# Performance work log

Measured on AMD Instinct MI355X. Metric: run time of the kernel, lower is better.

## Reference

```python
import jax, jax.numpy as jnp
import numpy as np

D = 1024   # dim_model
H = 16     # num_heads
DH = D // H  # per-head dim for k and v
B, S = 2, 2048
EPS = 1e-5


def layer_norm(x, g, b):
    mu = jnp.mean(x, axis=-1, keepdims=True)
    var = jnp.var(x, axis=-1, keepdims=True)
    return (x - mu) * jax.lax.rsqrt(var + EPS) * g + b


def setup_inputs() -> dict:
    key = jax.random.key(0)
    ks = jax.random.split(key, 8)
    s_d = 1.0 / np.sqrt(D)
    inp = {
        "x": jax.random.normal(ks[0], (B, S, D), dtype=jnp.float32),
        # stacked per-head projections, [H, D, DH] (torch Linear weight.T per head)
        "wq": jax.random.uniform(ks[1], (H, D, DH), jnp.float32, -s_d, s_d),
        "wk": jax.random.uniform(ks[2], (H, D, DH), jnp.float32, -s_d, s_d),
        "wv": jax.random.uniform(ks[3], (H, D, DH), jnp.float32, -s_d, s_d),
        "wo": jax.random.uniform(ks[4], (D, D), jnp.float32, -s_d, s_d),
        "w1": jax.random.uniform(ks[5], (D, D), jnp.float32, -s_d, s_d),  # FFN hidden == dim_model per source
        "w2": jax.random.uniform(ks[6], (D, D), jnp.float32, -s_d, s_d),
        "ln1_g": jnp.ones((D,), jnp.float32), "ln1_b": jnp.zeros((D,), jnp.float32),
        "ln2_g": jnp.ones((D,), jnp.float32), "ln2_b": jnp.zeros((D,), jnp.float32),
        "ln3_g": jnp.ones((D,), jnp.float32), "ln3_b": jnp.zeros((D,), jnp.float32),
    }
    return inp


def reference(x, wq, wk, wv, wo, w1, w2, ln1_g, ln1_b, ln2_g, ln2_b, ln3_g, ln3_b):
    residual = x
    h = layer_norm(x, ln1_g, ln1_b)  # pre_attention_norm
    # batched multi-head attention (equivalent to per-head loop + concat)
    q = jnp.einsum("bsd,hdk->bhsk", h, wq)
    k = jnp.einsum("bsd,hdk->bhsk", h, wk)
    v = jnp.einsum("bsd,hdk->bhsk", h, wv)
    scores = jnp.einsum("bhsk,bhtk->bhst", q, k) / jnp.sqrt(jnp.float32(DH))
    attn = jax.nn.softmax(scores, axis=-1)
    ctx = jnp.einsum("bhst,bhtk->bhsk", attn, v)        # [B,H,S,DH]
    concat = ctx.transpose(0, 2, 1, 3).reshape(x.shape[0], x.shape[1], -1)  # head concat order
    h = concat @ wo
    h = h + residual
    h = layer_norm(h, ln2_g, ln2_b)  # post_attention_norm (dropout is identity, rate=0)
    residual = h
    ffn = jnp.maximum(h @ w1, 0.0) @ w2
    h = ffn + residual
    h = layer_norm(h, ln3_g, ln3_b)  # post_ffn_norm
    return h
```

## Files before the change

### kernel.cpp

```cpp
#include <hip/hip_runtime.h>
#include <stdint.h>

typedef unsigned short u16;
typedef __attribute__((ext_vector_type(8))) short short8;
typedef __attribute__((ext_vector_type(4))) short short4v;
typedef __attribute__((ext_vector_type(4))) float f32x4;

#define DEV static __device__ __forceinline__

constexpr int DMODEL = 1024;
constexpr int SEQ = 2048;

DEV u16 f2b(float f){
  uint32_t u = __float_as_uint(f);
  u += 0x7FFF + ((u >> 16) & 1);
  return (u16)(u >> 16);
}

DEV float b2f(u16 b){ uint32_t u = ((uint32_t)b)<<16; return __uint_as_float(u); }

#define AS1(p) ((const __attribute__((address_space(1))) void*)(p))
#define AS3(p) ((__attribute__((address_space(3))) void*)(p))
#define GLOAD_LDS16(g, l) __builtin_amdgcn_global_load_lds(AS1(g), AS3(l), 16, 0, 0)
#define LDSADDR(p) ((uint32_t)(size_t)((__attribute__((address_space(3))) void*)(p)))

DEV short4v ds_tr16(uint32_t a){
  short4v r;
  asm volatile("ds_read_b64_tr_b16 %0, %1" : "=v"(r) : "v"(a) : "memory");
  return r;
}

DEV void pswap(uint32_t &a, uint32_t &b){
  asm("v_permlane32_swap_b32 %0, %1":"+v"(a),"+v"(b));
  asm("v_permlane16_swap_b32 %0, %1":"+v"(a),"+v"(b));
}

DEV uint32_t cvtpk(float lo, float hi){
  uint32_t r; asm("v_cvt_pk_bf16_f32 %0, %1, %2":"=v"(r):"v"(lo),"v"(hi)); return r;
}

__global__ __launch_bounds__(256) void transpose_all(
    const float* __restrict__ wq, const float* __restrict__ wk,
    const float* __restrict__ wv, const float* __restrict__ wo,
    const float* __restrict__ w1, const float* __restrict__ w2,
    u16* __restrict__ WqkvT, u16* __restrict__ WoT,
    u16* __restrict__ W1T, u16* __restrict__ W2T){
  __shared__ float tile[64][65];
  int bid = blockIdx.x;
  int j = threadIdx.x & 63, i0 = threadIdx.x >> 6;
  if(bid < 768){
    int xb = bid & 15, z = bid >> 4;
    int p = z >> 4, h = z & 15;
    const float* src = (p==0?wq:(p==1?wk:wv)) + (size_t)h*1024*64;
    float sc = (p==0) ? 0.18033688011112042f : 1.0f;
    int r0 = xb*64;
    for(int i=i0;i<64;i+=4) tile[i][j] = src[(size_t)(r0+i)*64 + j];
    __syncthreads();
    u16* drow = WqkvT + ((size_t)p*1024 + h*64)*1024;
    for(int jj=i0;jj<64;jj+=4) drow[(size_t)jj*1024 + r0 + j] = f2b(tile[j][jj]*sc);
  } else {
    int t = bid - 768;
    int which = t >> 8; t &= 255;
    const float* src = which==0?wo:(which==1?w1:w2);
    u16* dst = which==0?WoT:(which==1?W1T:W2T);
    int r0 = (t&15)*64, c0 = (t>>4)*64;
    for(int i=i0;i<64;i+=4) tile[i][j] = src[(size_t)(r0+i)*1024 + c0 + j];
    __syncthreads();
    for(int jj=i0;jj<64;jj+=4) dst[(size_t)(c0+jj)*1024 + r0 + j] = f2b(tile[j][jj]);
  }
}

__global__ __launch_bounds__(256) void ln_kernel(
    const float* __restrict__ in, const float* __restrict__ g, const float* __restrict__ bb,
    u16* __restrict__ outb, float* __restrict__ outf){
  int row = blockIdx.x, tid = threadIdx.x;
  const float4* x4 = (const float4*)(in + (size_t)row*DMODEL);
  float4 v = x4[tid];
  float s  = v.x+v.y+v.z+v.w;
  float ss = v.x*v.x + v.y*v.y + v.z*v.z + v.w*v.w;
  #pragma unroll
  for(int m=1;m<64;m<<=1){ s += __shfl_xor(s,m); ss += __shfl_xor(ss,m); }
  __shared__ float red[8];
  int w = tid>>6;
  if((tid&63)==0){ red[w]=s; red[4+w]=ss; }
  __syncthreads();
  s  = red[0]+red[1]+red[2]+red[3];
  ss = red[4]+red[5]+red[6]+red[7];
  float mu  = s*(1.f/DMODEL);
  float var = ss*(1.f/DMODEL) - mu*mu;
  float rs  = rsqrtf(var + 1e-5f);
  float4 gv = ((const float4*)g)[tid];
  float4 bv = ((const float4*)bb)[tid];
  float y0=(v.x-mu)*rs*gv.x+bv.x, y1=(v.y-mu)*rs*gv.y+bv.y;
  float y2=(v.z-mu)*rs*gv.z+bv.z, y3=(v.w-mu)*rs*gv.w+bv.w;
  if(outb){ ushort4 o = make_ushort4(f2b(y0),f2b(y1),f2b(y2),f2b(y3));
            ((ushort4*)outb)[(size_t)row*(DMODEL/4) + tid] = o; }
  if(outf){ ((float4*)outf)[(size_t)row*(DMODEL/4) + tid] = make_float4(y0,y1,y2,y3); }
}

template<int MODE>
__global__ __launch_bounds__(256) void gemm_bt(
    const u16* __restrict__ A, const u16* __restrict__ BT, int M, int N, int K,
    float* __restrict__ outf, u16* __restrict__ outb, const float* __restrict__ resf,
    const u16* __restrict__ resb){
  __shared__ u16 lsA[2][4096];
  __shared__ u16 lsB[2][4096];
  int n0 = blockIdx.x*128, m0 = blockIdx.y*128;
  int tid = threadIdx.x, lane = tid&63, w = tid>>6;
  int wr = w>>1, wc = w&1, rq = lane&15, hk = lane>>4;
  int o0 = tid*16, o1 = 4096 + tid*16;
  const u16* aS0 = A  + (size_t)(m0 + (o0>>6))*K + ((o0&63)>>1);
  const u16* aS1 = A  + (size_t)(m0 + (o1>>6))*K + ((o1&63)>>1);
  const u16* bS0 = BT + (size_t)(n0 + (o0>>6))*K + ((o0&63)>>1);
  const u16* bS1 = BT + (size_t)(n0 + (o1>>6))*K + ((o1&63)>>1);
  int nk = K>>5;
  f32x4 acc[4][4] = {};
  GLOAD_LDS16(aS0, &lsA[0][w*512]);
  GLOAD_LDS16(aS1, &lsA[0][2048 + w*512]);
  GLOAD_LDS16(bS0, &lsB[0][w*512]);
  GLOAD_LDS16(bS1, &lsB[0][2048 + w*512]);
  #pragma unroll 2
  for(int kt=0; kt<nk; ++kt){
    __syncthreads();
    if(kt+1 < nk){
      int nb = (kt+1)&1;
      GLOAD_LDS16(aS0 + (kt+1)*32, &lsA[nb][w*512]);
      GLOAD_LDS16(aS1 + (kt+1)*32, &lsA[nb][2048 + w*512]);
      GLOAD_LDS16(bS0 + (kt+1)*32, &lsB[nb][w*512]);
      GLOAD_LDS16(bS1 + (kt+1)*32, &lsB[nb][2048 + w*512]);
    }
    const u16* la = &lsA[kt&1][0];
    const u16* lb = &lsB[kt&1][0];
    short8 aF[4], bF[4];
    #pragma unroll
    for(int m=0;m<4;++m) aF[m] = *(const short8*)(la + (wr*64 + m*16 + rq)*32 + hk*8);
    #pragma unroll
    for(int n=0;n<4;++n) bF[n] = *(const short8*)(lb + (wc*64 + n*16 + rq)*32 + hk*8);
    __builtin_amdgcn_s_setprio(1);
    #pragma unroll
    for(int m=0;m<4;++m){
      #pragma unroll
      for(int n=0;n<4;++n)
        acc[m][n] = __builtin_amdgcn_mfma_f32_16x16x32_bf16(aF[m], bF[n], acc[m][n], 0,0,0);
    }
    __builtin_amdgcn_s_setprio(0);
  }
  #pragma unroll
  for(int m=0;m<4;++m){
    #pragma unroll
    for(int n=0;n<4;++n){
      int rb = m0 + wr*64 + m*16 + (hk<<2);
      int c  = n0 + wc*64 + n*16 + rq;
      #pragma unroll
      for(int qq=0;qq<4;++qq){
        int r = rb+qq; float val = acc[m][n][qq];
        if constexpr(MODE==2){
          outf[(size_t)r*N + c] = val + resf[(size_t)r*N + c];
        } else if constexpr(MODE==3){
          outb[(size_t)r*N + c] = f2b(val>0.f?val:0.f);
        } else if constexpr(MODE==4){
          outf[(size_t)r*N + c] = val + b2f(resb[(size_t)r*N + c]);
        } else {
          outb[(size_t)r*N + c] = f2b(val);
        }
      }
    }
  }
}

__global__ __launch_bounds__(128) void attn_kernel(
    const u16* __restrict__ qkv, u16* __restrict__ concat){
  __shared__ u16 lsK[2][4096];
  __shared__ u16 lsV[2][4096];
  int qt = blockIdx.x, bh = blockIdx.y;
  int b = bh>>4, h = bh&15;
  const u16* qp = qkv + (size_t)b*2048*3072 + h*64;
  const u16* kp = qp + 1024;
  const u16* vp = qp + 2048;
  int tid=threadIdx.x, lane=tid&63, w=tid>>6;
  int rq = lane&15, hk = lane>>4;
  const uint32_t sw = (uint32_t)((rq&7)<<4);

  short8 aQ[2][2];
  #pragma unroll
  for(int qg=0;qg<2;++qg){
    const u16* qrow = qp + (size_t)(qt*64 + w*32 + qg*16 + rq)*3072 + hk*8;
    aQ[qg][0] = *(const short8*)(qrow);
    aQ[qg][1] = *(const short8*)(qrow + 32);
  }
  short8 bOnes;
  #pragma unroll
  for(int j=0;j<8;++j) bOnes[j] = (short)0x3F80;

  const u16* kS[4]; const u16* vS[4];
  #pragma unroll
  for(int i=0;i<4;++i){
    int c = i*128 + tid;
    int o = c*16;
    int krow = o>>7;
    kS[i] = kp + (size_t)krow*3072 + ((((o&127) ^ ((krow&7)<<4)))>>1);
    int vt = ((c>>5)<<2)|((c&7)>>1);
    int vd8 = (((c>>3)&3)<<1)|(c&1);
    vS[i] = vp + (size_t)vt*3072 + vd8*8;
  }
  const size_t TS = (size_t)64*3072;

  f32x4 accO[2][4] = {};
  f32x4 accL[2] = {};

  #pragma unroll
  for(int i=0;i<4;++i){
    GLOAD_LDS16(kS[i], &lsK[0][i*1024 + w*512]);
    GLOAD_LDS16(vS[i], &lsV[0][i*1024 + w*512]);
  }

  int cur = 0;
  for(int kt=0; kt<SEQ/64; ++kt){
    __syncthreads();
    if(kt+1 < SEQ/64){
      int nb = cur^1;
      #pragma unroll
      for(int i=0;i<4;++i){
        GLOAD_LDS16(kS[i] + (kt+1)*TS, &lsK[nb][i*1024 + w*512]);
        GLOAD_LDS16(vS[i] + (kt+1)*TS, &lsV[nb][i*1024 + w*512]);
      }
    }
    const char* kb = (const char*)&lsK[cur][0];
    uint32_t apk[2][2][4];
    #pragma unroll
    for(int tp=0; tp<2; ++tp){
      short8 bK[2][2];
      #pragma unroll
      for(int t2=0;t2<2;++t2){
        uint32_t rb = (uint32_t)(((tp*2+t2)*16+rq)*128);
        bK[t2][0] = *(const short8*)(kb + rb + (((uint32_t)(hk<<4)) ^ sw));
        bK[t2][1] = *(const short8*)(kb + rb + ((64u|(uint32_t)(hk<<4)) ^ sw));
      }
      f32x4 z[2][2];
      __builtin_amdgcn_s_setprio(1);
      #pragma unroll
      for(int qg=0;qg<2;++qg){
        #pragma unroll
        for(int t2=0;t2<2;++t2){
          f32x4 zz = {};
          zz = __builtin_amdgcn_mfma_f32_16x16x32_bf16(bK[t2][0], aQ[qg][0], zz, 0,0,0);
          zz = __builtin_amdgcn_mfma_f32_16x16x32_bf16(bK[t2][1], aQ[qg][1], zz, 0,0,0);
          z[qg][t2] = zz;
        }
      }
      __builtin_amdgcn_s_setprio(0);
      #pragma unroll
      for(int qg=0;qg<2;++qg){
        #pragma unroll
        for(int t2=0;t2<2;++t2){
          #pragma unroll
          for(int r=0;r<4;++r) z[qg][t2][r] = __builtin_exp2f(z[qg][t2][r]);
        }
        uint32_t a0=cvtpk(z[qg][0][0],z[qg][0][1]), a1=cvtpk(z[qg][0][2],z[qg][0][3]);
        uint32_t b0=cvtpk(z[qg][1][0],z[qg][1][1]), b1=cvtpk(z[qg][1][2],z[qg][1][3]);
        pswap(a0,b0); pswap(a1,b1);
        apk[tp][qg][0]=a0; apk[tp][qg][1]=a1; apk[tp][qg][2]=b0; apk[tp][qg][3]=b1;
      }
    }
    uint32_t vA = LDSADDR(&lsV[cur][0]) + (uint32_t)(hk*1024 + rq*2);
    short4v vL[2][4][2];
    #pragma unroll
    for(int kh=0;kh<2;++kh){
      #pragma unroll
      for(int ds=0;ds<4;++ds){
        vL[kh][ds][0] = ds_tr16(vA + kh*4096 + ds*128);
        vL[kh][ds][1] = ds_tr16(vA + kh*4096 + ds*128 + 512);
      }
    }
    asm volatile("s_waitcnt lgkmcnt(0)" ::: "memory");
    __builtin_amdgcn_sched_barrier(0);
    __builtin_amdgcn_s_setprio(1);
    #pragma unroll
    for(int kh=0;kh<2;++kh){
      #pragma unroll
      for(int qg=0;qg<2;++qg){
        union U8 { uint32_t d[4]; short8 v; } ap;
        ap.d[0]=apk[kh][qg][0]; ap.d[1]=apk[kh][qg][1];
        ap.d[2]=apk[kh][qg][2]; ap.d[3]=apk[kh][qg][3];
        accL[qg] = __builtin_amdgcn_mfma_f32_16x16x32_bf16(ap.v, bOnes, accL[qg], 0,0,0);
        #pragma unroll
        for(int ds=0;ds<4;++ds){
          short8 bV = __builtin_shufflevector(vL[kh][ds][0], vL[kh][ds][1], 0,1,2,3,4,5,6,7);
          accO[qg][ds] = __builtin_amdgcn_mfma_f32_16x16x32_bf16(ap.v, bV, accO[qg][ds], 0,0,0);
        }
      }
    }
    __builtin_amdgcn_s_setprio(0);
    cur ^= 1;
  }
  #pragma unroll
  for(int qg=0;qg<2;++qg){
    #pragma unroll
    for(int r=0;r<4;++r){
      float inv = 1.f / accL[qg][r];
      int si = qt*64 + w*32 + qg*16 + hk*4 + r;
      #pragma unroll
      for(int ds=0;ds<4;++ds){
        int c = h*64 + ds*16 + rq;
        concat[((size_t)b*SEQ + si)*DMODEL + c] = f2b(accO[qg][ds][r] * inv);
      }
    }
  }
}

extern "C" void kernel_launch(void* const* d_in, const int* in_sizes, int n_in,
                              void* d_out, int out_size, void* d_ws, size_t ws_size,
                              hipStream_t stream){
  (void)in_sizes; (void)n_in; (void)out_size; (void)ws_size;
  const float* x    = (const float*)d_in[0];
  const float* wq   = (const float*)d_in[1];
  const float* wk   = (const float*)d_in[2];
  const float* wv   = (const float*)d_in[3];
  const float* wo   = (const float*)d_in[4];
  const float* w1   = (const float*)d_in[5];
  const float* w2   = (const float*)d_in[6];
  const float* ln1g = (const float*)d_in[7];
  const float* ln1b = (const float*)d_in[8];
  const float* ln2g = (const float*)d_in[9];
  const float* ln2b = (const float*)d_in[10];
  const float* ln3g = (const float*)d_in[11];
  const float* ln3b = (const float*)d_in[12];
  float* out = (float*)d_out;

  char* ws = (char*)d_ws; size_t off = 0;
  auto alloc = [&](size_t b)->char*{ char* p = ws + off; off += (b + 255) & ~(size_t)255; return p; };
  u16*   WqkvT = (u16*)  alloc((size_t)3072*1024*2);
  u16*   WoT   = (u16*)  alloc((size_t)1024*1024*2);
  u16*   W1T   = (u16*)  alloc((size_t)1024*1024*2);
  u16*   W2T   = (u16*)  alloc((size_t)1024*1024*2);
  u16*   h1    = (u16*)  alloc((size_t)4096*1024*2);
  u16*   qkv   = (u16*)  alloc((size_t)4096*3072*2);
  u16*   cc    = (u16*)  alloc((size_t)4096*1024*2);
  float* r1    = (float*)alloc((size_t)4096*1024*4);
  u16*   h2b   = (u16*)  alloc((size_t)4096*1024*2);
  float* r2    = (float*)alloc((size_t)4096*1024*4);
  u16*   ffn1  = h1;

  transpose_all<<<1536,256,0,stream>>>(wq,wk,wv,wo,w1,w2, WqkvT,WoT,W1T,W2T);

  ln_kernel<<<4096,256,0,stream>>>(x, ln1g, ln1b, h1, nullptr);
  gemm_bt<0><<<dim3(24,32),256,0,stream>>>(h1,WqkvT,4096,3072,1024,
      nullptr,qkv,nullptr,nullptr);
  attn_kernel<<<dim3(32,32),128,0,stream>>>(qkv,cc);
  gemm_bt<2><<<dim3(8,32),256,0,stream>>>(cc,WoT,4096,1024,1024,
      r1,nullptr,x,nullptr);
  ln_kernel<<<4096,256,0,stream>>>(r1, ln2g, ln2b, h2b, nullptr);
  gemm_bt<3><<<dim3(8,32),256,0,stream>>>(h2b,W1T,4096,1024,1024,
      nullptr,ffn1,nullptr,nullptr);
  gemm_bt<4><<<dim3(8,32),256,0,stream>>>(ffn1,W2T,4096,1024,1024,
      r2,nullptr,nullptr,h2b);
  ln_kernel<<<4096,256,0,stream>>>(r2, ln3g, ln3b, nullptr, out);
}
```

Measured before the change: 211.9 us.

## Split attention block into four waves of sixteen query rows each

The attention kernel now runs 256 threads (4 waves) per 64-query block, and each wave handles 16 query rows instead of 32. The K/V tile loads into LDS are spread across more threads, and the LDS base addresses are precomputed per buffer. The exp/pack work is moved after the V transpose reads are issued so it can overlap them. This raises per-block parallelism and lowers register pressure, at the cost of each wave reading the full K/V tile from LDS for fewer query rows, which means more LDS traffic per unit of work.

After: 226.6 us. 6.9% more time.

```diff
diff --git a/kernel.cpp b/kernel.cpp
--- a/kernel.cpp
+++ b/kernel.cpp
@@ -168,7 +168,7 @@
   }
 }
 
-__global__ __launch_bounds__(128) void attn_kernel(
+__global__ __launch_bounds__(256) void attn_kernel(
     const u16* __restrict__ qkv, u16* __restrict__ concat){
   __shared__ u16 lsK[2][4096];
   __shared__ u16 lsV[2][4096];
@@ -181,88 +181,70 @@
   int rq = lane&15, hk = lane>>4;
   const uint32_t sw = (uint32_t)((rq&7)<<4);
 
-  short8 aQ[2][2];
-  #pragma unroll
-  for(int qg=0;qg<2;++qg){
-    const u16* qrow = qp + (size_t)(qt*64 + w*32 + qg*16 + rq)*3072 + hk*8;
-    aQ[qg][0] = *(const short8*)(qrow);
-    aQ[qg][1] = *(const short8*)(qrow + 32);
+  short8 aQ[2];
+  {
+    const u16* qrow = qp + (size_t)(qt*64 + w*16 + rq)*3072 + hk*8;
+    aQ[0] = *(const short8*)(qrow);
+    aQ[1] = *(const short8*)(qrow + 32);
   }
   short8 bOnes;
   #pragma unroll
   for(int j=0;j<8;++j) bOnes[j] = (short)0x3F80;
 
-  const u16* kS[4]; const u16* vS[4];
-  #pragma unroll
-  for(int i=0;i<4;++i){
-    int c = i*128 + tid;
-    int o = c*16;
-    int krow = o>>7;
-    kS[i] = kp + (size_t)krow*3072 + ((((o&127) ^ ((krow&7)<<4)))>>1);
-    int vt = ((c>>5)<<2)|((c&7)>>1);
-    int vd8 = (((c>>3)&3)<<1)|(c&1);
-    vS[i] = vp + (size_t)vt*3072 + vd8*8;
-  }
+  int o0 = tid*16,        kr0 = o0>>7;
+  int o1 = 4096 + tid*16, kr1 = o1>>7;
+  const u16* kS0 = kp + (size_t)kr0*3072 + ((((o0&127) ^ ((kr0&7)<<4)))>>1);
+  const u16* kS1 = kp + (size_t)kr1*3072 + ((((o1&127) ^ ((kr1&7)<<4)))>>1);
+  int c0v = tid,      vt0 = ((c0v>>5)<<2)|((c0v&7)>>1), vd0 = (((c0v>>3)&3)<<1)|(c0v&1);
+  int c1v = 256+tid,  vt1 = ((c1v>>5)<<2)|((c1v&7)>>1), vd1 = (((c1v>>3)&3)<<1)|(c1v&1);
+  const u16* vS0 = vp + (size_t)vt0*3072 + vd0*8;
+  const u16* vS1 = vp + (size_t)vt1*3072 + vd1*8;
   const size_t TS = (size_t)64*3072;
 
-  f32x4 accO[2][4] = {};
-  f32x4 accL[2] = {};
-
-  #pragma unroll
-  for(int i=0;i<4;++i){
-    GLOAD_LDS16(kS[i], &lsK[0][i*1024 + w*512]);
-    GLOAD_LDS16(vS[i], &lsV[0][i*1024 + w*512]);
-  }
+  const uint32_t xo0 = ((uint32_t)(hk<<4) ^ sw) + (uint32_t)(rq*128);
+  const uint32_t xo1 = ((64u|(uint32_t)(hk<<4)) ^ sw) + (uint32_t)(rq*128);
+  const char* kb0[2] = { (const char*)&lsK[0][0] + xo0, (const char*)&lsK[1][0] + xo0 };
+  const char* kb1[2] = { (const char*)&lsK[0][0] + xo1, (const char*)&lsK[1][0] + xo1 };
+  const uint32_t voffs = (uint32_t)(hk*1024 + rq*2);
+  const uint32_t vbase[2] = { LDSADDR(&lsV[0][0]) + voffs, LDSADDR(&lsV[1][0]) + voffs };
+
+  f32x4 accO[4] = {};
+  f32x4 accL = {};
+
+  GLOAD_LDS16(kS0, &lsK[0][w*512]);
+  GLOAD_LDS16(kS1, &lsK[0][2048+w*512]);
+  GLOAD_LDS16(vS0, &lsV[0][w*512]);
+  GLOAD_LDS16(vS1, &lsV[0][2048+w*512]);
 
   int cur = 0;
   for(int kt=0; kt<SEQ/64; ++kt){
     __syncthreads();
     if(kt+1 < SEQ/64){
       int nb = cur^1;
-      #pragma unroll
-      for(int i=0;i<4;++i){
-        GLOAD_LDS16(kS[i] + (kt+1)*TS, &lsK[nb][i*1024 + w*512]);
-        GLOAD_LDS16(vS[i] + (kt+1)*TS, &lsV[nb][i*1024 + w*512]);
-      }
-    }
-    const char* kb = (const char*)&lsK[cur][0];
-    uint32_t apk[2][2][4];
-    #pragma unroll
-    for(int tp=0; tp<2; ++tp){
-      short8 bK[2][2];
-      #pragma unroll
-      for(int t2=0;t2<2;++t2){
-        uint32_t rb = (uint32_t)(((tp*2+t2)*16+rq)*128);
-        bK[t2][0] = *(const short8*)(kb + rb + (((uint32_t)(hk<<4)) ^ sw));
-        bK[t2][1] = *(const short8*)(kb + rb + ((64u|(uint32_t)(hk<<4)) ^ sw));
-      }
-      f32x4 z[2][2];
-      __builtin_amdgcn_s_setprio(1);
-      #pragma unroll
-      for(int qg=0;qg<2;++qg){
-        #pragma unroll
-        for(int t2=0;t2<2;++t2){
-          f32x4 zz = {};
-          zz = __builtin_amdgcn_mfma_f32_16x16x32_bf16(bK[t2][0], aQ[qg][0], zz, 0,0,0);
-          zz = __builtin_amdgcn_mfma_f32_16x16x32_bf16(bK[t2][1], aQ[qg][1], zz, 0,0,0);
-          z[qg][t2] = zz;
-        }
-      }
-      __builtin_amdgcn_s_setprio(0);
-      #pragma unroll
-      for(int qg=0;qg<2;++qg){
-        #pragma unroll
-        for(int t2=0;t2<2;++t2){
-          #pragma unroll
-          for(int r=0;r<4;++r) z[qg][t2][r] = __builtin_exp2f(z[qg][t2][r]);
-        }
-        uint32_t a0=cvtpk(z[qg][0][0],z[qg][0][1]), a1=cvtpk(z[qg][0][2],z[qg][0][3]);
-        uint32_t b0=cvtpk(z[qg][1][0],z[qg][1][1]), b1=cvtpk(z[qg][1][2],z[qg][1][3]);
-        pswap(a0,b0); pswap(a1,b1);
-        apk[tp][qg][0]=a0; apk[tp][qg][1]=a1; apk[tp][qg][2]=b0; apk[tp][qg][3]=b1;
-      }
-    }
-    uint32_t vA = LDSADDR(&lsV[cur][0]) + (uint32_t)(hk*1024 + rq*2);
+      GLOAD_LDS16(kS0 + (kt+1)*TS, &lsK[nb][w*512]);
+      GLOAD_LDS16(kS1 + (kt+1)*TS, &lsK[nb][2048+w*512]);
+      GLOAD_LDS16(vS0 + (kt+1)*TS, &lsV[nb][w*512]);
+      GLOAD_LDS16(vS1 + (kt+1)*TS, &lsV[nb][2048+w*512]);
+    }
+    const char* k0 = kb0[cur];
+    const char* k1 = kb1[cur];
+    short8 bK[4][2];
+    #pragma unroll
+    for(int ts=0;ts<4;++ts){
+      bK[ts][0] = *(const short8*)(k0 + ts*2048);
+      bK[ts][1] = *(const short8*)(k1 + ts*2048);
+    }
+    f32x4 z[4];
+    __builtin_amdgcn_s_setprio(1);
+    #pragma unroll
+    for(int ts=0;ts<4;++ts){
+      f32x4 zz = {};
+      zz = __builtin_amdgcn_mfma_f32_16x16x32_bf16(bK[ts][0], aQ[0], zz, 0,0,0);
+      zz = __builtin_amdgcn_mfma_f32_16x16x32_bf16(bK[ts][1], aQ[1], zz, 0,0,0);
+      z[ts] = zz;
+    }
+    __builtin_amdgcn_s_setprio(0);
+    uint32_t vA = vbase[cur];
     short4v vL[2][4][2];
     #pragma unroll
     for(int kh=0;kh<2;++kh){
@@ -272,38 +254,45 @@
         vL[kh][ds][1] = ds_tr16(vA + kh*4096 + ds*128 + 512);
       }
     }
+    #pragma unroll
+    for(int ts=0;ts<4;++ts){
+      #pragma unroll
+      for(int r=0;r<4;++r)
+        z[ts][r] = __builtin_exp2f(z[ts][r]);
+    }
+    uint32_t u00=cvtpk(z[0][0],z[0][1]), u01=cvtpk(z[0][2],z[0][3]);
+    uint32_t u10=cvtpk(z[1][0],z[1][1]), u11=cvtpk(z[1][2],z[1][3]);
+    uint32_t u20=cvtpk(z[2][0],z[2][1]), u21=cvtpk(z[2][2],z[2][3]);
+    uint32_t u30=cvtpk(z[3][0],z[3][1]), u31=cvtpk(z[3][2],z[3][3]);
+    pswap(u00,u10); pswap(u01,u11);
+    pswap(u20,u30); pswap(u21,u31);
+    union U8 { uint32_t d[4]; short8 v; } ap0, ap1;
+    ap0.d[0]=u00; ap0.d[1]=u01; ap0.d[2]=u10; ap0.d[3]=u11;
+    ap1.d[0]=u20; ap1.d[1]=u21; ap1.d[2]=u30; ap1.d[3]=u31;
     asm volatile("s_waitcnt lgkmcnt(0)" ::: "memory");
     __builtin_amdgcn_sched_barrier(0);
     __builtin_amdgcn_s_setprio(1);
     #pragma unroll
     for(int kh=0;kh<2;++kh){
-      #pragma unroll
-      for(int qg=0;qg<2;++qg){
-        union U8 { uint32_t d[4]; short8 v; } ap;
-        ap.d[0]=apk[kh][qg][0]; ap.d[1]=apk[kh][qg][1];
-        ap.d[2]=apk[kh][qg][2]; ap.d[3]=apk[kh][qg][3];
-        accL[qg] = __builtin_amdgcn_mfma_f32_16x16x32_bf16(ap.v, bOnes, accL[qg], 0,0,0);
-        #pragma unroll
-        for(int ds=0;ds<4;++ds){
-          short8 bV = __builtin_shufflevector(vL[kh][ds][0], vL[kh][ds][1], 0,1,2,3,4,5,6,7);
-          accO[qg][ds] = __builtin_amdgcn_mfma_f32_16x16x32_bf16(ap.v, bV, accO[qg][ds], 0,0,0);
-        }
+      short8 aP = kh ? ap1.v : ap0.v;
+      accL = __builtin_amdgcn_mfma_f32_16x16x32_bf16(aP, bOnes, accL, 0,0,0);
+      #pragma unroll
+      for(int ds=0;ds<4;++ds){
+        short8 bV = __builtin_shufflevector(vL[kh][ds][0], vL[kh][ds][1], 0,1,2,3,4,5,6,7);
+        accO[ds] = __builtin_amdgcn_mfma_f32_16x16x32_bf16(aP, bV, accO[ds], 0,0,0);
       }
     }
     __builtin_amdgcn_s_setprio(0);
     cur ^= 1;
   }
   #pragma unroll
-  for(int qg=0;qg<2;++qg){
-    #pragma unroll
-    for(int r=0;r<4;++r){
-      float inv = 1.f / accL[qg][r];
-      int si = qt*64 + w*32 + qg*16 + hk*4 + r;
-      #pragma unroll
-      for(int ds=0;ds<4;++ds){
-        int c = h*64 + ds*16 + rq;
-        concat[((size_t)b*SEQ + si)*DMODEL + c] = f2b(accO[qg][ds][r] * inv);
-      }
+  for(int r=0;r<4;++r){
+    float inv = 1.f / accL[r];
+    int si = qt*64 + w*16 + hk*4 + r;
+    #pragma unroll
+    for(int ds=0;ds<4;++ds){
+      int c = h*64 + ds*16 + rq;
+      concat[((size_t)b*SEQ + si)*DMODEL + c] = f2b(accO[ds][r] * inv);
     }
   }
 }
@@ -346,7 +335,7 @@
   ln_kernel<<<4096,256,0,stream>>>(x, ln1g, ln1b, h1, nullptr);
   gemm_bt<0><<<dim3(24,32),256,0,stream>>>(h1,WqkvT,4096,3072,1024,
       nullptr,qkv,nullptr,nullptr);
-  attn_kernel<<<dim3(32,32),128,0,stream>>>(qkv,cc);
+  attn_kernel<<<dim3(32,32),256,0,stream>>>(qkv,cc);
   gemm_bt<2><<<dim3(8,32),256,0,stream>>>(cc,WoT,4096,1024,1024,
       r1,nullptr,x,nullptr);
   ln_kernel<<<4096,256,0,stream>>>(r1, ln2g, ln2b, h2b, nullptr);
```
